# Optimization experiments

Hardware: AMD Instinct MI355X
Metric: run time of the kernel (lower is better)

The kernel has to match this reference:

```python
import jax, jax.numpy as jnp
import numpy as np

E, L, D, H, S, B = 8, 12, 768, 12, 512, 32
DIMS = [12, 8, 8, 8, 8, 12]
RANKS = [1, 8, 8, 8, 8, 8, 1]
ALPHA = 8.0


def setup_inputs() -> dict:
    key = jax.random.key(0)
    ks = iter(jax.random.split(key, 32))
    inp = {}
    inp['hidden_states'] = jax.random.normal(next(ks), (B, S, D), jnp.float32)
    inp['router_weights'] = jax.random.normal(next(ks), (D, E), jnp.float32)
    for pre in ('q', 'v'):
        for i in range(6):
            shp = (E, L, RANKS[i], DIMS[i], RANKS[i + 1])
            inp[f'{pre}_core{i}'] = jax.random.normal(next(ks), shp, jnp.float32) * 0.05
    for nm in ('Wq', 'Wk', 'Wv', 'Wo'):
        inp[nm] = jax.random.normal(next(ks), (L, D, D), jnp.float32) * 0.02
    for nm in ('bq', 'bk', 'bv', 'bo'):
        inp[nm] = jnp.zeros((L, D), jnp.float32)
    inp['ln_scale'] = jnp.ones((L, D), jnp.float32)
    inp['ln_bias'] = jnp.zeros((L, D), jnp.float32)
    return inp


def _layernorm(x, scale, bias, eps=1e-12):
    mu = x.mean(-1, keepdims=True)
    var = ((x - mu) ** 2).mean(-1, keepdims=True)
    return (x - mu) * jax.lax.rsqrt(var + eps) * scale + bias


def _tt_weights(cores):
    # cores[i]: [L, r_i, d_i, r_{i+1}]; chained TT contraction, vectorized over layers
    w = jnp.einsum('Lijk,Lklm,Lmno,Lopq,Lqrs,Lstu->Ljlnprt', *cores)
    return w.reshape(w.shape[0], D, D)  # [L, out, in] (matches torch weight.reshape)


def reference(hidden_states, router_weights,
              q_core0, q_core1, q_core2, q_core3, q_core4, q_core5,
              v_core0, v_core1, v_core2, v_core3, v_core4, v_core5,
              Wq, Wk, Wv, Wo, bq, bk, bv, bo, ln_scale, ln_bias):
    # routing: pool over sequence, softmax + argmax per sample
    pooled = hidden_states.mean(axis=1)                      # [B, D]
    probs = jax.nn.softmax(pooled @ router_weights, axis=-1)  # [B, E]
    idx = jnp.argmax(probs, axis=-1)                          # [B]
    e = idx[-1]
    qc = [c[e] for c in (q_core0, q_core1, q_core2, q_core3, q_core4, q_core5)]
    vc = [c[e] for c in (v_core0, v_core1, v_core2, v_core3, v_core4, v_core5)]
    Wq_a = Wq + ALPHA * _tt_weights(qc)  # [L, D, D]
    Wv_a = Wv + ALPHA * _tt_weights(vc)

    hd = D // H
    scale = 1.0 / jnp.sqrt(jnp.float32(hd))
    x = hidden_states
    for l in range(L):
        q = (x @ Wq_a[l].T + bq[l]).reshape(B, S, H, hd)
        k = (x @ Wk[l].T + bk[l]).reshape(B, S, H, hd)
        v = (x @ Wv_a[l].T + bv[l]).reshape(B, S, H, hd)
        scores = jnp.einsum('bqhd,bkhd->bhqk', q, k) * scale
        attn = jax.nn.softmax(scores, axis=-1)
        ctx = jnp.einsum('bhqk,bkhd->bqhd', attn, v).reshape(B, S, D)
        out = ctx @ Wo[l].T + bo[l]
        x = _layernorm(x + out, ln_scale[l], ln_bias[l])
    return x
```

## Files before the change

### kernel.cpp

```cpp
#include <hip/hip_runtime.h>
#include <hip/hip_bf16.h>
#include <stdint.h>

#define E_ 8
#define L_ 12
#define D_ 768
#define H_ 12
#define S_ 512
#define B_ 32
#define BS_ (B_*S_)

typedef __attribute__((ext_vector_type(4))) float floatx4;
typedef __attribute__((ext_vector_type(8))) __bf16 bf16x8;
typedef __attribute__((ext_vector_type(4))) __bf16 bf16x4;

__device__ __forceinline__ __bf16 f2bf(float f) {
  unsigned u = __builtin_bit_cast(unsigned, f);
  u += 0x7fffu + ((u >> 16) & 1u);
  unsigned short h = (unsigned short)(u >> 16);
  return __builtin_bit_cast(__bf16, h);
}

__device__ __forceinline__ float fexp2(float x) {
#if __has_builtin(__builtin_amdgcn_exp2f)
  return __builtin_amdgcn_exp2f(x);
#else
  return exp2f(x);
#endif
}

__device__ __forceinline__ void async16(const void* g, void* l) {
  __builtin_amdgcn_global_load_lds((__attribute__((address_space(1))) void*)g,
                                   (__attribute__((address_space(3))) void*)l,
                                   16, 0, 0);
}

__global__ void routing_pool_kernel(const float* __restrict__ hidden,
                                    float* __restrict__ partial) {
  const int blk = blockIdx.x;
  const int tid = threadIdx.x;
  const float* base = hidden + (size_t)(B_-1)*S_*D_ + (size_t)blk*8*D_;
  float acc[3] = {0.f, 0.f, 0.f};
  for (int s = 0; s < 8; ++s) {
#pragma unroll
    for (int i = 0; i < 3; ++i)
      acc[i] += base[(size_t)s*D_ + tid + i*256];
  }
#pragma unroll
  for (int i = 0; i < 3; ++i) partial[(size_t)blk*D_ + tid + i*256] = acc[i];
}

__global__ void routing_finish_kernel(const float* __restrict__ partial,
                                      const float* __restrict__ rw,
                                      int* __restrict__ e_out) {
  __shared__ float pooled[D_];
  __shared__ float logits[E_];
  int tid = threadIdx.x;
#pragma unroll
  for (int i = 0; i < 3; ++i) {
    int d = tid + i*256;
    float s = 0.f;
    for (int blk = 0; blk < 64; ++blk) s += partial[(size_t)blk*D_ + d];
    pooled[d] = s;
  }
  __syncthreads();
  if (tid < E_) {
    float s = 0.f;
    for (int d = 0; d < D_; ++d) s += pooled[d] * rw[d*E_ + tid];
    logits[tid] = s;
  }
  __syncthreads();
  if (tid == 0) {
    int best = 0; float bvv = logits[0];
    for (int e = 1; e < E_; ++e) if (logits[e] > bvv) { bvv = logits[e]; best = e; }
    e_out[0] = best;
  }
}

__global__ void convert_bf16_kernel(const float* __restrict__ src, __bf16* __restrict__ dst) {
  size_t i = ((size_t)blockIdx.x*256 + threadIdx.x)*8;
  __bf16 r[8];
#pragma unroll
  for (int j = 0; j < 8; ++j) r[j] = f2bf(src[i+j]);
  *(bf16x8*)(dst + i) = *(bf16x8*)r;
}

__global__ void convert_wk_kernel(const float* __restrict__ wk, __bf16* __restrict__ wqkv) {
  size_t i = ((size_t)blockIdx.x*256 + threadIdx.x)*8;
  int l = (int)(i / (D_*D_));
  int rem = (int)(i % (D_*D_));
  int n = rem / D_, k = rem % D_;
  __bf16 r[8];
#pragma unroll
  for (int j = 0; j < 8; ++j) r[j] = f2bf(wk[i+j]);
  *(bf16x8*)(wqkv + (size_t)l*2304*D_ + (size_t)(768+n)*D_ + k) = *(bf16x8*)r;
}

__global__ void tt_prep_kernel(
    const float* __restrict__ qc0, const float* __restrict__ qc1, const float* __restrict__ qc2,
    const float* __restrict__ qc3, const float* __restrict__ qc4, const float* __restrict__ qc5,
    const float* __restrict__ vc0, const float* __restrict__ vc1, const float* __restrict__ vc2,
    const float* __restrict__ vc3, const float* __restrict__ vc4, const float* __restrict__ vc5,
    const float* __restrict__ Wq, const float* __restrict__ Wv,
    const int* __restrict__ e_idx, __bf16* __restrict__ wqkv) {
  const int l = blockIdx.x;
  const int pre = blockIdx.y;
  const int z = blockIdx.z;
  const int tid = threadIdx.x;
  const int e = e_idx[0];
  const float* c0 = (pre ? vc0 : qc0) + (size_t)(e*L_ + l)*96;
  const float* c1 = (pre ? vc1 : qc1) + (size_t)(e*L_ + l)*512;
  const float* c2 = (pre ? vc2 : qc2) + (size_t)(e*L_ + l)*512;
  const float* c3 = (pre ? vc3 : qc3) + (size_t)(e*L_ + l)*512;
  const float* c4 = (pre ? vc4 : qc4) + (size_t)(e*L_ + l)*512;
  const float* c5 = (pre ? vc5 : qc5) + (size_t)(e*L_ + l)*96;
  __shared__ float M1[768];
  __shared__ float R2[768];
  __shared__ float M2[6144];
  __shared__ float Rm[6144];
  for (int idx = tid; idx < 768; idx += 256) {
    int j = idx >> 6, rem = idx & 63, l2 = rem >> 3, m = rem & 7;
    float s = 0.f;
    for (int k = 0; k < 8; ++k) s += c0[j*8 + k] * c1[k*64 + l2*8 + m];
    M1[idx] = s;
    int qq = idx / 96, rem2 = idx % 96, rr = rem2 / 12, t = rem2 % 12;
    float s2 = 0.f;
    for (int si = 0; si < 8; ++si) s2 += c4[qq*64 + rr*8 + si] * c5[si*12 + t];
    R2[idx] = s2;
  }
  __syncthreads();
  for (int idx = tid; idx < 6144; idx += 256) {
    int o = idx & 7, n = (idx >> 3) & 7, jl = idx >> 6;
    float s = 0.f;
    for (int m = 0; m < 8; ++m) s += M1[jl*8 + m] * c2[m*64 + n*8 + o];
    M2[idx] = s;
    int o2 = idx / 768, inp = idx % 768, p = inp / 96, rt = inp % 96;
    float s2 = 0.f;
    for (int qq = 0; qq < 8; ++qq) s2 += c3[o2*64 + p*8 + qq] * R2[qq*96 + rt];
    Rm[idx] = s2;
  }
  __syncthreads();
  const float* Wbase = (pre ? Wv : Wq) + (size_t)l*D_*D_;
  __bf16* dst = wqkv + (size_t)l*2304*D_ + (pre ? (size_t)1536*D_ : 0);
  for (int g = tid; g < 48*96; g += 256) {
    const int outr = z*48 + (g / 96);
    const int inp0 = (g % 96) * 8;
    float m2r[8];
#pragma unroll
    for (int o = 0; o < 8; ++o) m2r[o] = M2[outr*8 + o];
    float acc[8];
#pragma unroll
    for (int u = 0; u < 8; ++u) acc[u] = 0.f;
#pragma unroll
    for (int o = 0; o < 8; ++o) {
      float4 r0 = *(const float4*)&Rm[o*768 + inp0];
      float4 r1 = *(const float4*)&Rm[o*768 + inp0 + 4];
      acc[0] += m2r[o]*r0.x; acc[1] += m2r[o]*r0.y;
      acc[2] += m2r[o]*r0.z; acc[3] += m2r[o]*r0.w;
      acc[4] += m2r[o]*r1.x; acc[5] += m2r[o]*r1.y;
      acc[6] += m2r[o]*r1.z; acc[7] += m2r[o]*r1.w;
    }
    const float* wb = Wbase + (size_t)outr*768 + inp0;
    float4 w0 = *(const float4*)wb;
    float4 w1 = *(const float4*)(wb + 4);
    __bf16 r[8];
    r[0] = f2bf(w0.x + 8.f*acc[0]); r[1] = f2bf(w0.y + 8.f*acc[1]);
    r[2] = f2bf(w0.z + 8.f*acc[2]); r[3] = f2bf(w0.w + 8.f*acc[3]);
    r[4] = f2bf(w1.x + 8.f*acc[4]); r[5] = f2bf(w1.y + 8.f*acc[5]);
    r[6] = f2bf(w1.z + 8.f*acc[6]); r[7] = f2bf(w1.w + 8.f*acc[7]);
    *(bf16x8*)(dst + (size_t)outr*768 + inp0) = *(bf16x8*)r;
  }
}

#define SLOT_BYTES 28672
template<bool SPLITV>
__global__ __launch_bounds__(512, 2) void gemm_bt(
    const __bf16* __restrict__ A, const __bf16* __restrict__ Bw,
    const float* __restrict__ bq, const float* __restrict__ bk, const float* __restrict__ bvp,
    __bf16* __restrict__ outb, __bf16* __restrict__ vtout, int Nw) {
  __shared__ __align__(16) char lds[4*SLOT_BYTES];
  const int tid = threadIdx.x;
  const int w = tid >> 6, lane = tid & 63;
  const int quad = lane >> 4, l16 = lane & 15;
  const int wm = w >> 2, wn = w & 3;
  const size_t mblk = (size_t)blockIdx.y * 256;
  const size_t nblk = (size_t)blockIdx.x * 192;
  const __bf16* Ag = A + mblk * 768;
  const __bf16* Bg = Bw + nblk * 768;

  int a_goff[2], a_loff[2];
#pragma unroll
  for (int i = 0; i < 2; ++i) {
    int line = w*16 + i*8 + (lane >> 3);
    int s8 = (lane & 7) ^ (line & 7);
    int row = 2*line + (s8 >> 2);
    a_goff[i] = row*768 + (s8 & 3)*8;
    a_loff[i] = (w*16 + i*8)*128;
  }
  int b_goff[2], b_loff[2];
#pragma unroll
  for (int i = 0; i < 2; ++i) {
    int bl0 = (w < 4) ? (w*16 + i*8) : (64 + (w-4)*8);
    int line = bl0 + (lane >> 3);
    int s8 = (lane & 7) ^ (line & 7);
    int row = 2*line + (s8 >> 2);
    b_goff[i] = row*768 + (s8 & 3)*8;
    b_loff[i] = 16384 + bl0*128;
  }

  int a_foff[8], b_foff[3];
#pragma unroll
  for (int mf = 0; mf < 8; ++mf) {
    int r = wm*128 + mf*16 + l16;
    int line = r >> 1, s8 = (r & 1)*4 + quad, ph = s8 ^ (line & 7);
    a_foff[mf] = line*128 + ph*16;
  }
#pragma unroll
  for (int nf = 0; nf < 3; ++nf) {
    int r = wn*48 + nf*16 + l16;
    int line = r >> 1, s8 = (r & 1)*4 + quad, ph = s8 ^ (line & 7);
    b_foff[nf] = 16384 + line*128 + ph*16;
  }

  floatx4 acc[8][3];
#pragma unroll
  for (int mf = 0; mf < 8; ++mf)
#pragma unroll
    for (int nf = 0; nf < 3; ++nf) acc[mf][nf] = {0.f,0.f,0.f,0.f};

  auto STAGE = [&](int t) {
    const __bf16* Ab = Ag + t*32;
    const __bf16* Bb = Bg + t*32;
    char* ls = lds + (t & 3)*SLOT_BYTES;
    async16(Ab + a_goff[0], ls + a_loff[0]);
    async16(Ab + a_goff[1], ls + a_loff[1]);
    if (w < 4) {
      async16(Bb + b_goff[0], ls + b_loff[0]);
      async16(Bb + b_goff[1], ls + b_loff[1]);
    } else {
      async16(Bb + b_goff[0], ls + b_loff[0]);
    }
  };

  bf16x8 af[8], bfr[3];
  auto LOAD1 = [&](int u) {
    const char* ls = lds + (u & 3)*SLOT_BYTES;
#pragma unroll
    for (int nf = 0; nf < 3; ++nf) bfr[nf] = *(const bf16x8*)(ls + b_foff[nf]);
#pragma unroll
    for (int mf = 0; mf < 4; ++mf) af[mf] = *(const bf16x8*)(ls + a_foff[mf]);
  };
  auto LOAD2 = [&](int u) {
    const char* ls = lds + (u & 3)*SLOT_BYTES;
#pragma unroll
    for (int mf = 4; mf < 8; ++mf) af[mf] = *(const bf16x8*)(ls + a_foff[mf]);
  };
  auto MM = [&](int mf0) {
    __builtin_amdgcn_s_setprio(1);
#pragma unroll
    for (int mf = mf0; mf < mf0 + 4; ++mf)
#pragma unroll
      for (int nf = 0; nf < 3; ++nf)
        acc[mf][nf] = __builtin_amdgcn_mfma_f32_16x16x32_bf16(af[mf], bfr[nf], acc[mf][nf], 0, 0, 0);
    __builtin_amdgcn_s_setprio(0);
  };
  auto BAR = [&]() {
    __builtin_amdgcn_s_barrier();
    __builtin_amdgcn_sched_barrier(0);
  };

  STAGE(0); STAGE(1); STAGE(2);
  if (w < 4) asm volatile("s_waitcnt vmcnt(8)" ::: "memory");
  else       asm volatile("s_waitcnt vmcnt(6)" ::: "memory");
  BAR();

  for (int u = 0; u < 21; ++u) {
    LOAD1(u);
    BAR();
    MM(0);
    LOAD2(u);
    STAGE(u + 3);
    if (w < 4) asm volatile("s_waitcnt vmcnt(8)" ::: "memory");
    else       asm volatile("s_waitcnt vmcnt(6)" ::: "memory");
    BAR();
    MM(4);
  }
  LOAD1(21);
  BAR();
  MM(0);
  LOAD2(21);
  if (w < 4) asm volatile("s_waitcnt vmcnt(4)" ::: "memory");
  else       asm volatile("s_waitcnt vmcnt(3)" ::: "memory");
  BAR();
  MM(4);
  LOAD1(22);
  BAR();
  MM(0);
  LOAD2(22);
  asm volatile("s_waitcnt vmcnt(0)" ::: "memory");
  BAR();
  MM(4);
  LOAD1(23);
  BAR();
  MM(0);
  LOAD2(23);
  BAR();
  MM(4);

  if (SPLITV && blockIdx.x >= 8) {
#pragma unroll
    for (int nf = 0; nf < 3; ++nf) {
      const int vcol = (int)nblk - 1536 + wn*48 + nf*16 + l16;
      const int h = vcol >> 6, d = vcol & 63;
      const float bval = bvp[vcol];
#pragma unroll
      for (int mf = 0; mf < 8; ++mf) {
        const int mrow = (int)mblk + wm*128 + mf*16 + quad*4;
        const int b = mrow >> 9, s = mrow & 511;
        __bf16 pr[4];
#pragma unroll
        for (int r = 0; r < 4; ++r) pr[r] = f2bf(acc[mf][nf][r] + bval);
        *(bf16x4*)(vtout + (size_t)((b*H_ + h)*64 + d)*S_ + s) = *(bf16x4*)pr;
      }
    }
    return;
  }
  const float* bias = bq;
  if (SPLITV) bias = (blockIdx.x < 4) ? bq : bk;
  float bval[3]; int ncol[3];
#pragma unroll
  for (int nf = 0; nf < 3; ++nf) {
    ncol[nf] = (int)nblk + wn*48 + nf*16 + l16;
    int bc = ncol[nf]; if (bc >= 768) bc -= 768;
    bval[nf] = bias[bc];
  }
#pragma unroll
  for (int mf = 0; mf < 8; ++mf) {
#pragma unroll
    for (int nf = 0; nf < 3; ++nf) {
#pragma unroll
      for (int r = 0; r < 4; ++r) {
        const int mrow = (int)mblk + wm*128 + mf*16 + quad*4 + r;
        outb[(size_t)mrow*Nw + ncol[nf]] = f2bf(acc[mf][nf][r] + bval[nf]);
      }
    }
  }
}

#define PSTR 72
__global__ __launch_bounds__(256) void flash_kernel(const __bf16* __restrict__ qkv,
                                                    const __bf16* __restrict__ vt,
                                                    __bf16* __restrict__ ctx) {
  __shared__ __align__(16) __bf16 Qs[64*PSTR];
  __shared__ __align__(16) __bf16 Ks[64*PSTR];
  __shared__ __align__(16) __bf16 Vts[64*PSTR];
  __shared__ __align__(16) __bf16 Ps[64*PSTR];
  const int tid = threadIdx.x;
  const int w = tid >> 6, lane = tid & 63;
  const int quad = lane >> 4, l16 = lane & 15;
  const int n = blockIdx.x;
  const int bh = (n >> 6)*8 + (n & 7);
  const int q0 = ((n >> 3) & 7) * 64;
  const int b = bh / H_, h = bh % H_;
  const float SCL = 0.125f * 1.44269504f;

  const int row0 = tid >> 3,        seg0 = tid & 7;
  const int row1 = (256 + tid) >> 3, seg1 = tid & 7;

  bf16x8 ka[2], va[2], kb[2], vb[2];
  ka[0] = *(const bf16x8*)(qkv + (size_t)(b*S_ + row0)*2304 + 768 + h*64 + seg0*8);
  va[0] = *(const bf16x8*)(vt  + (size_t)(bh*64 + row0)*S_ + seg0*8);
  ka[1] = *(const bf16x8*)(qkv + (size_t)(b*S_ + row1)*2304 + 768 + h*64 + seg1*8);
  va[1] = *(const bf16x8*)(vt  + (size_t)(bh*64 + row1)*S_ + seg1*8);

  {
    bf16x8 v0 = *(const bf16x8*)(qkv + (size_t)(b*S_ + q0 + row0)*2304 + h*64 + seg0*8);
    bf16x8 v1 = *(const bf16x8*)(qkv + (size_t)(b*S_ + q0 + row1)*2304 + h*64 + seg1*8);
    *(bf16x8*)&Qs[row0*PSTR + seg0*8] = v0;
    *(bf16x8*)&Qs[row1*PSTR + seg1*8] = v1;
  }

  floatx4 acc_o[4];
#pragma unroll
  for (int jd = 0; jd < 4; ++jd) acc_o[jd] = {0.f,0.f,0.f,0.f};
  float m_prev = -__builtin_inff();
  float l_part = 0.f;

  auto STEP = [&](int kt, bf16x8* ck, bf16x8* cv, bf16x8* nk, bf16x8* nv, bool pf) {
    asm volatile("s_waitcnt lgkmcnt(0)" ::: "memory");
    __builtin_amdgcn_s_barrier();
    __builtin_amdgcn_sched_barrier(0);
    *(bf16x8*)&Ks[row0*PSTR + seg0*8]  = ck[0];
    *(bf16x8*)&Vts[row0*PSTR + seg0*8] = cv[0];
    *(bf16x8*)&Ks[row1*PSTR + seg1*8]  = ck[1];
    *(bf16x8*)&Vts[row1*PSTR + seg1*8] = cv[1];
    if (pf) {
      nk[0] = *(const bf16x8*)(qkv + (size_t)(b*S_ + (kt+1)*64 + row0)*2304 + 768 + h*64 + seg0*8);
      nv[0] = *(const bf16x8*)(vt  + (size_t)(bh*64 + row0)*S_ + (kt+1)*64 + seg0*8);
      nk[1] = *(const bf16x8*)(qkv + (size_t)(b*S_ + (kt+1)*64 + row1)*2304 + 768 + h*64 + seg1*8);
      nv[1] = *(const bf16x8*)(vt  + (size_t)(bh*64 + row1)*S_ + (kt+1)*64 + seg1*8);
    }
    asm volatile("s_waitcnt lgkmcnt(0)" ::: "memory");
    __builtin_amdgcn_s_barrier();
    __builtin_amdgcn_sched_barrier(0);

    floatx4 sacc[4];
#pragma unroll
    for (int i = 0; i < 4; ++i) sacc[i] = {0.f,0.f,0.f,0.f};
    __builtin_amdgcn_s_setprio(1);
#pragma unroll
    for (int kk = 0; kk < 64; kk += 32) {
      bf16x8 bq_ = *(const bf16x8*)&Qs[(w*16 + l16)*PSTR + kk + quad*8];
#pragma unroll
      for (int i = 0; i < 4; ++i) {
        bf16x8 ak = *(const bf16x8*)&Ks[(i*16 + l16)*PSTR + kk + quad*8];
        sacc[i] = __builtin_amdgcn_mfma_f32_16x16x32_bf16(ak, bq_, sacc[i], 0, 0, 0);
      }
    }
    __builtin_amdgcn_s_setprio(0);
#pragma unroll
    for (int i = 0; i < 4; ++i)
#pragma unroll
      for (int r = 0; r < 4; ++r) sacc[i][r] *= SCL;
    float mloc = sacc[0][0];
#pragma unroll
    for (int i = 0; i < 4; ++i)
#pragma unroll
      for (int r = 0; r < 4; ++r) mloc = fmaxf(mloc, sacc[i][r]);
    mloc = fmaxf(mloc, __shfl_xor(mloc, 16));
    mloc = fmaxf(mloc, __shfl_xor(mloc, 32));
    float mnew = fmaxf(m_prev, mloc);
    float alpha = fexp2(m_prev - mnew);
    m_prev = mnew;
    float rsum = 0.f;
#pragma unroll
    for (int i = 0; i < 4; ++i) {
      __bf16 pr[4];
#pragma unroll
      for (int r = 0; r < 4; ++r) {
        float p = fexp2(sacc[i][r] - mnew);
        rsum += p;
        pr[r] = f2bf(p);
      }
      *(bf16x4*)&Ps[(w*16 + l16)*PSTR + i*16 + quad*4] = *(bf16x4*)pr;
    }
    l_part = l_part*alpha + rsum;
    float ab[4];
#pragma unroll
    for (int r = 0; r < 4; ++r) ab[r] = __shfl(alpha, quad*4 + r);
#pragma unroll
    for (int jd = 0; jd < 4; ++jd)
#pragma unroll
      for (int r = 0; r < 4; ++r) acc_o[jd][r] *= ab[r];
#pragma unroll
    for (int kk = 0; kk < 64; kk += 32) {
      bf16x8 ap = *(const bf16x8*)&Ps[(w*16 + l16)*PSTR + kk + quad*8];
      __builtin_amdgcn_s_setprio(1);
#pragma unroll
      for (int jd = 0; jd < 4; ++jd) {
        bf16x8 bv_ = *(const bf16x8*)&Vts[(jd*16 + l16)*PSTR + kk + quad*8];
        acc_o[jd] = __builtin_amdgcn_mfma_f32_16x16x32_bf16(ap, bv_, acc_o[jd], 0, 0, 0);
      }
      __builtin_amdgcn_s_setprio(0);
    }
  };

#pragma unroll
  for (int kt2 = 0; kt2 < 8; kt2 += 2) {
    STEP(kt2,     ka, va, kb, vb, true);
    STEP(kt2 + 1, kb, vb, ka, va, kt2 + 1 < 7);
  }

  float l_tot = l_part;
  l_tot += __shfl_xor(l_tot, 16);
  l_tot += __shfl_xor(l_tot, 32);
  float lb[4];
#pragma unroll
  for (int r = 0; r < 4; ++r) lb[r] = __shfl(l_tot, quad*4 + r);
#pragma unroll
  for (int jd = 0; jd < 4; ++jd) {
    const int d = jd*16 + l16;
#pragma unroll
    for (int r = 0; r < 4; ++r) {
      const int q = q0 + w*16 + quad*4 + r;
      ctx[(size_t)(b*S_ + q)*D_ + h*64 + d] = f2bf(acc_o[jd][r] / lb[r]);
    }
  }
}

template<bool FIRST, bool LAST>
__global__ __launch_bounds__(256) void ln_kernel(const float* __restrict__ residf,
                                                 __bf16* xb,
                                                 const __bf16* __restrict__ proj,
                                                 const float* __restrict__ gamma,
                                                 const float* __restrict__ beta,
                                                 float* __restrict__ xoutf) {
  const int tid = threadIdx.x;
  const int w = tid >> 6, lane = tid & 63;
  const int row = blockIdx.x*4 + w;
  const size_t base = (size_t)row * D_;
  const int c0 = lane*8;
  const bool has2 = lane < 32;
  const int c1 = 512 + lane*8;

  float v0[8], v1[8];
  {
    bf16x8 p0 = *(const bf16x8*)(proj + base + c0);
    if (FIRST) {
      float4 a = *(const float4*)(residf + base + c0);
      float4 bq4 = *(const float4*)(residf + base + c0 + 4);
      v0[0]=a.x+(float)p0[0]; v0[1]=a.y+(float)p0[1]; v0[2]=a.z+(float)p0[2]; v0[3]=a.w+(float)p0[3];
      v0[4]=bq4.x+(float)p0[4]; v0[5]=bq4.y+(float)p0[5]; v0[6]=bq4.z+(float)p0[6]; v0[7]=bq4.w+(float)p0[7];
    } else {
      bf16x8 r0 = *(const bf16x8*)(xb + base + c0);
#pragma unroll
      for (int j = 0; j < 8; ++j) v0[j] = (float)r0[j] + (float)p0[j];
    }
    if (has2) {
      bf16x8 p1 = *(const bf16x8*)(proj + base + c1);
      if (FIRST) {
        float4 a = *(const float4*)(residf + base + c1);
        float4 bq4 = *(const float4*)(residf + base + c1 + 4);
        v1[0]=a.x+(float)p1[0]; v1[1]=a.y+(float)p1[1]; v1[2]=a.z+(float)p1[2]; v1[3]=a.w+(float)p1[3];
        v1[4]=bq4.x+(float)p1[4]; v1[5]=bq4.y+(float)p1[5]; v1[6]=bq4.z+(float)p1[6]; v1[7]=bq4.w+(float)p1[7];
      } else {
        bf16x8 r1 = *(const bf16x8*)(xb + base + c1);
#pragma unroll
        for (int j = 0; j < 8; ++j) v1[j] = (float)r1[j] + (float)p1[j];
      }
    } else {
#pragma unroll
      for (int j = 0; j < 8; ++j) v1[j] = 0.f;
    }
  }
  float s = 0.f;
#pragma unroll
  for (int j = 0; j < 8; ++j) s += v0[j] + v1[j];
#pragma unroll
  for (int off = 32; off; off >>= 1) s += __shfl_xor(s, off);
  const float mu = s * (1.f/768.f);
  float q = 0.f;
#pragma unroll
  for (int j = 0; j < 8; ++j) { float d0 = v0[j]-mu; q += d0*d0; }
  if (has2) {
#pragma unroll
    for (int j = 0; j < 8; ++j) { float d1 = v1[j]-mu; q += d1*d1; }
  }
#pragma unroll
  for (int off = 32; off; off >>= 1) q += __shfl_xor(q, off);
  const float rs = rsqrtf(q * (1.f/768.f) + 1e-12f);

  {
    float4 g0 = *(const float4*)(gamma + c0);
    float4 g1 = *(const float4*)(gamma + c0 + 4);
    float4 b0 = *(const float4*)(beta + c0);
    float4 b1 = *(const float4*)(beta + c0 + 4);
    float o[8];
    o[0]=(v0[0]-mu)*rs*g0.x+b0.x; o[1]=(v0[1]-mu)*rs*g0.y+b0.y;
    o[2]=(v0[2]-mu)*rs*g0.z+b0.z; o[3]=(v0[3]-mu)*rs*g0.w+b0.w;
    o[4]=(v0[4]-mu)*rs*g1.x+b1.x; o[5]=(v0[5]-mu)*rs*g1.y+b1.y;
    o[6]=(v0[6]-mu)*rs*g1.z+b1.z; o[7]=(v0[7]-mu)*rs*g1.w+b1.w;
    if (LAST) {
      *(float4*)(xoutf + base + c0)     = {o[0],o[1],o[2],o[3]};
      *(float4*)(xoutf + base + c0 + 4) = {o[4],o[5],o[6],o[7]};
    } else {
      __bf16 ob[8];
#pragma unroll
      for (int j = 0; j < 8; ++j) ob[j] = f2bf(o[j]);
      *(bf16x8*)(xb + base + c0) = *(bf16x8*)ob;
    }
  }
  if (has2) {
    float4 g0 = *(const float4*)(gamma + c1);
    float4 g1 = *(const float4*)(gamma + c1 + 4);
    float4 b0 = *(const float4*)(beta + c1);
    float4 b1 = *(const float4*)(beta + c1 + 4);
    float o[8];
    o[0]=(v1[0]-mu)*rs*g0.x+b0.x; o[1]=(v1[1]-mu)*rs*g0.y+b0.y;
    o[2]=(v1[2]-mu)*rs*g0.z+b0.z; o[3]=(v1[3]-mu)*rs*g0.w+b0.w;
    o[4]=(v1[4]-mu)*rs*g1.x+b1.x; o[5]=(v1[5]-mu)*rs*g1.y+b1.y;
    o[6]=(v1[6]-mu)*rs*g1.z+b1.z; o[7]=(v1[7]-mu)*rs*g1.w+b1.w;
    if (LAST) {
      *(float4*)(xoutf + base + c1)     = {o[0],o[1],o[2],o[3]};
      *(float4*)(xoutf + base + c1 + 4) = {o[4],o[5],o[6],o[7]};
    } else {
      __bf16 ob[8];
#pragma unroll
      for (int j = 0; j < 8; ++j) ob[j] = f2bf(o[j]);
      *(bf16x8*)(xb + base + c1) = *(bf16x8*)ob;
    }
  }
}

extern "C" void kernel_launch(void* const* d_in, const int* in_sizes, int n_in,
                              void* d_out, int out_size, void* d_ws, size_t ws_size,
                              hipStream_t stream) {
  const float* hidden = (const float*)d_in[0];
  const float* router = (const float*)d_in[1];
  const float* qc[6]; const float* vc[6];
  for (int i = 0; i < 6; ++i) qc[i] = (const float*)d_in[2+i];
  for (int i = 0; i < 6; ++i) vc[i] = (const float*)d_in[8+i];
  const float* Wq = (const float*)d_in[14];
  const float* Wk = (const float*)d_in[15];
  const float* Wv = (const float*)d_in[16];
  const float* Wo = (const float*)d_in[17];
  const float* bq = (const float*)d_in[18];
  const float* bk = (const float*)d_in[19];
  const float* bv = (const float*)d_in[20];
  const float* bo = (const float*)d_in[21];
  const float* lns = (const float*)d_in[22];
  const float* lnb = (const float*)d_in[23];
  float* out = (float*)d_out;

  char* ws = (char*)d_ws;
  size_t off = 0;
  auto alloc = [&](size_t bytes) -> void* {
    off = (off + 255) & ~(size_t)255;
    void* p = ws + off; off += bytes; return p;
  };
  int*    e_idx = (int*)   alloc(4);
  float*  rpart = (float*) alloc((size_t)64*D_*4);
  __bf16* xbf   = (__bf16*)alloc((size_t)BS_*D_*2);
  __bf16* qkv   = (__bf16*)alloc((size_t)BS_*2304*2);
  __bf16* vt    = (__bf16*)alloc((size_t)B_*H_*64*S_*2);
  __bf16* ctx   = (__bf16*)alloc((size_t)BS_*D_*2);
  __bf16* projb = (__bf16*)alloc((size_t)BS_*D_*2);
  __bf16* wqkv  = (__bf16*)alloc((size_t)L_*2304*D_*2);
  __bf16* wobf  = (__bf16*)alloc((size_t)L_*D_*D_*2);
  (void)ws_size; (void)in_sizes; (void)n_in; (void)out_size;

  routing_pool_kernel<<<64, 256, 0, stream>>>(hidden, rpart);
  routing_finish_kernel<<<1, 256, 0, stream>>>(rpart, router, e_idx);
  convert_bf16_kernel<<<(BS_*D_)/2048, 256, 0, stream>>>(hidden, xbf);
  tt_prep_kernel<<<dim3(L_, 2, 16), 256, 0, stream>>>(qc[0],qc[1],qc[2],qc[3],qc[4],qc[5],
                                                      vc[0],vc[1],vc[2],vc[3],vc[4],vc[5],
                                                      Wq, Wv, e_idx, wqkv);
  convert_wk_kernel<<<(L_*D_*D_)/2048, 256, 0, stream>>>(Wk, wqkv);
  convert_bf16_kernel<<<(L_*D_*D_)/2048, 256, 0, stream>>>(Wo, wobf);

  for (int l = 0; l < L_; ++l) {
    gemm_bt<true><<<dim3(12,64), 512, 0, stream>>>(xbf, wqkv + (size_t)l*2304*D_,
        bq + l*D_, bk + l*D_, bv + l*D_, qkv, vt, 2304);
    flash_kernel<<<3072, 256, 0, stream>>>(qkv, vt, ctx);
    gemm_bt<false><<<dim3(4,64), 512, 0, stream>>>(ctx, wobf + (size_t)l*D_*D_,
        bo + l*D_, nullptr, nullptr, projb, nullptr, 768);
    if (l == 0)
      ln_kernel<true,false><<<BS_/4, 256, 0, stream>>>(hidden, xbf, projb,
          lns + l*D_, lnb + l*D_, nullptr);
    else if (l == L_-1)
      ln_kernel<false,true><<<BS_/4, 256, 0, stream>>>(nullptr, xbf, projb,
          lns + l*D_, lnb + l*D_, out);
    else
      ln_kernel<false,false><<<BS_/4, 256, 0, stream>>>(nullptr, xbf, projb,
          lns + l*D_, lnb + l*D_, nullptr);
  }
}
```

Measured before the change: 2.446 ms.

## Keep Q in registers and skip online-softmax rescale when max barely grows

The flash attention kernel now holds Q fragments in registers instead of shared memory. It skips the running-max rescale of the output accumulator unless some row's max grows by more than a threshold (FA4-style lazy rescaling). The change also packs P to bf16 with v_cvt_pk_bf16_f32, uses incrementing prefetch pointers, multiplies by a reciprocal at the end, and sets launch bounds for 4 blocks per CU. The intent is to cut LDS traffic, exp and multiply work, and raise occupancy, at the cost of exponents up to 2^10 before normalization and a different rounding mode for the conversion.

Result: faster. 2.254 ms (-7.9%).

```diff
diff --git a/kernel.cpp b/kernel.cpp
--- a/kernel.cpp
+++ b/kernel.cpp
@@ -13,12 +13,19 @@
 typedef __attribute__((ext_vector_type(4))) float floatx4;
 typedef __attribute__((ext_vector_type(8))) __bf16 bf16x8;
 typedef __attribute__((ext_vector_type(4))) __bf16 bf16x4;
+typedef __attribute__((ext_vector_type(2))) unsigned uintx2;
 
 __device__ __forceinline__ __bf16 f2bf(float f) {
   unsigned u = __builtin_bit_cast(unsigned, f);
   u += 0x7fffu + ((u >> 16) & 1u);
   unsigned short h = (unsigned short)(u >> 16);
   return __builtin_bit_cast(__bf16, h);
+}
+
+__device__ __forceinline__ unsigned cvtpk_bf16(float lo, float hi) {
+  unsigned r;
+  asm("v_cvt_pk_bf16_f32 %0, %1, %2" : "=v"(r) : "v"(lo), "v"(hi));
+  return r;
 }
 
 __device__ __forceinline__ float fexp2(float x) {
@@ -348,10 +355,9 @@
 }
 
 #define PSTR 72
-__global__ __launch_bounds__(256) void flash_kernel(const __bf16* __restrict__ qkv,
-                                                    const __bf16* __restrict__ vt,
-                                                    __bf16* __restrict__ ctx) {
-  __shared__ __align__(16) __bf16 Qs[64*PSTR];
+__global__ __launch_bounds__(256, 4) void flash_kernel(const __bf16* __restrict__ qkv,
+                                                       const __bf16* __restrict__ vt,
+                                                       __bf16* __restrict__ ctx) {
   __shared__ __align__(16) __bf16 Ks[64*PSTR];
   __shared__ __align__(16) __bf16 Vts[64*PSTR];
   __shared__ __align__(16) __bf16 Ps[64*PSTR];
@@ -364,7 +370,7 @@
   const int b = bh / H_, h = bh % H_;
   const float SCL = 0.125f * 1.44269504f;
 
-  const int row0 = tid >> 3,        seg0 = tid & 7;
+  const int row0 = tid >> 3,         seg0 = tid & 7;
   const int row1 = (256 + tid) >> 3, seg1 = tid & 7;
 
   bf16x8 ka[2], va[2], kb[2], vb[2];
@@ -373,12 +379,17 @@
   ka[1] = *(const bf16x8*)(qkv + (size_t)(b*S_ + row1)*2304 + 768 + h*64 + seg1*8);
   va[1] = *(const bf16x8*)(vt  + (size_t)(bh*64 + row1)*S_ + seg1*8);
 
+  bf16x8 qf0, qf1;
   {
-    bf16x8 v0 = *(const bf16x8*)(qkv + (size_t)(b*S_ + q0 + row0)*2304 + h*64 + seg0*8);
-    bf16x8 v1 = *(const bf16x8*)(qkv + (size_t)(b*S_ + q0 + row1)*2304 + h*64 + seg1*8);
-    *(bf16x8*)&Qs[row0*PSTR + seg0*8] = v0;
-    *(bf16x8*)&Qs[row1*PSTR + seg1*8] = v1;
-  }
+    const __bf16* qrow = qkv + (size_t)(b*S_ + q0 + w*16 + l16)*2304 + h*64 + quad*8;
+    qf0 = *(const bf16x8*)qrow;
+    qf1 = *(const bf16x8*)(qrow + 32);
+  }
+
+  const __bf16* kp0 = qkv + (size_t)(b*S_ + 64 + row0)*2304 + 768 + h*64 + seg0*8;
+  const __bf16* kp1 = qkv + (size_t)(b*S_ + 64 + row1)*2304 + 768 + h*64 + seg1*8;
+  const __bf16* vp0 = vt  + (size_t)(bh*64 + row0)*S_ + 64 + seg0*8;
+  const __bf16* vp1 = vt  + (size_t)(bh*64 + row1)*S_ + 64 + seg1*8;
 
   floatx4 acc_o[4];
 #pragma unroll
@@ -386,7 +397,7 @@
   float m_prev = -__builtin_inff();
   float l_part = 0.f;
 
-  auto STEP = [&](int kt, bf16x8* ck, bf16x8* cv, bf16x8* nk, bf16x8* nv, bool pf) {
+  auto STEP = [&](bf16x8* ck, bf16x8* cv, bf16x8* nk, bf16x8* nv, bool pf) {
     asm volatile("s_waitcnt lgkmcnt(0)" ::: "memory");
     __builtin_amdgcn_s_barrier();
     __builtin_amdgcn_sched_barrier(0);
@@ -395,10 +406,10 @@
     *(bf16x8*)&Ks[row1*PSTR + seg1*8]  = ck[1];
     *(bf16x8*)&Vts[row1*PSTR + seg1*8] = cv[1];
     if (pf) {
-      nk[0] = *(const bf16x8*)(qkv + (size_t)(b*S_ + (kt+1)*64 + row0)*2304 + 768 + h*64 + seg0*8);
-      nv[0] = *(const bf16x8*)(vt  + (size_t)(bh*64 + row0)*S_ + (kt+1)*64 + seg0*8);
-      nk[1] = *(const bf16x8*)(qkv + (size_t)(b*S_ + (kt+1)*64 + row1)*2304 + 768 + h*64 + seg1*8);
-      nv[1] = *(const bf16x8*)(vt  + (size_t)(bh*64 + row1)*S_ + (kt+1)*64 + seg1*8);
+      nk[0] = *(const bf16x8*)kp0; kp0 += 64*2304;
+      nv[0] = *(const bf16x8*)vp0; vp0 += 64;
+      nk[1] = *(const bf16x8*)kp1; kp1 += 64*2304;
+      nv[1] = *(const bf16x8*)vp1; vp1 += 64;
     }
     asm volatile("s_waitcnt lgkmcnt(0)" ::: "memory");
     __builtin_amdgcn_s_barrier();
@@ -410,7 +421,7 @@
     __builtin_amdgcn_s_setprio(1);
 #pragma unroll
     for (int kk = 0; kk < 64; kk += 32) {
-      bf16x8 bq_ = *(const bf16x8*)&Qs[(w*16 + l16)*PSTR + kk + quad*8];
+      bf16x8 bq_ = kk ? qf1 : qf0;
 #pragma unroll
       for (int i = 0; i < 4; ++i) {
         bf16x8 ak = *(const bf16x8*)&Ks[(i*16 + l16)*PSTR + kk + quad*8];
@@ -429,29 +440,33 @@
       for (int r = 0; r < 4; ++r) mloc = fmaxf(mloc, sacc[i][r]);
     mloc = fmaxf(mloc, __shfl_xor(mloc, 16));
     mloc = fmaxf(mloc, __shfl_xor(mloc, 32));
-    float mnew = fmaxf(m_prev, mloc);
-    float alpha = fexp2(m_prev - mnew);
-    m_prev = mnew;
+    const bool resc = !__all(mloc <= m_prev + 10.f);
+    float mnew = m_prev;
+    if (resc) mnew = fmaxf(m_prev, mloc);
     float rsum = 0.f;
 #pragma unroll
     for (int i = 0; i < 4; ++i) {
-      __bf16 pr[4];
-#pragma unroll
-      for (int r = 0; r < 4; ++r) {
-        float p = fexp2(sacc[i][r] - mnew);
-        rsum += p;
-        pr[r] = f2bf(p);
-      }
-      *(bf16x4*)&Ps[(w*16 + l16)*PSTR + i*16 + quad*4] = *(bf16x4*)pr;
-    }
-    l_part = l_part*alpha + rsum;
-    float ab[4];
-#pragma unroll
-    for (int r = 0; r < 4; ++r) ab[r] = __shfl(alpha, quad*4 + r);
-#pragma unroll
-    for (int jd = 0; jd < 4; ++jd)
-#pragma unroll
-      for (int r = 0; r < 4; ++r) acc_o[jd][r] *= ab[r];
+      float p0 = fexp2(sacc[i][0] - mnew);
+      float p1 = fexp2(sacc[i][1] - mnew);
+      float p2 = fexp2(sacc[i][2] - mnew);
+      float p3 = fexp2(sacc[i][3] - mnew);
+      rsum += (p0 + p1) + (p2 + p3);
+      uintx2 pk = { cvtpk_bf16(p0, p1), cvtpk_bf16(p2, p3) };
+      *(uintx2*)&Ps[(w*16 + l16)*PSTR + i*16 + quad*4] = pk;
+    }
+    if (resc) {
+      float alpha = fexp2(m_prev - mnew);
+      m_prev = mnew;
+      l_part *= alpha;
+      float ab[4];
+#pragma unroll
+      for (int r = 0; r < 4; ++r) ab[r] = __shfl(alpha, quad*4 + r);
+#pragma unroll
+      for (int jd = 0; jd < 4; ++jd)
+#pragma unroll
+        for (int r = 0; r < 4; ++r) acc_o[jd][r] *= ab[r];
+    }
+    l_part += rsum;
 #pragma unroll
     for (int kk = 0; kk < 64; kk += 32) {
       bf16x8 ap = *(const bf16x8*)&Ps[(w*16 + l16)*PSTR + kk + quad*8];
@@ -467,8 +482,8 @@
 
 #pragma unroll
   for (int kt2 = 0; kt2 < 8; kt2 += 2) {
-    STEP(kt2,     ka, va, kb, vb, true);
-    STEP(kt2 + 1, kb, vb, ka, va, kt2 + 1 < 7);
+    STEP(ka, va, kb, vb, true);
+    STEP(kb, vb, ka, va, kt2 + 1 < 7);
   }
 
   float l_tot = l_part;
@@ -476,14 +491,14 @@
   l_tot += __shfl_xor(l_tot, 32);
   float lb[4];
 #pragma unroll
-  for (int r = 0; r < 4; ++r) lb[r] = __shfl(l_tot, quad*4 + r);
+  for (int r = 0; r < 4; ++r) lb[r] = 1.f / __shfl(l_tot, quad*4 + r);
 #pragma unroll
   for (int jd = 0; jd < 4; ++jd) {
     const int d = jd*16 + l16;
 #pragma unroll
     for (int r = 0; r < 4; ++r) {
       const int q = q0 + w*16 + quad*4 + r;
-      ctx[(size_t)(b*S_ + q)*D_ + h*64 + d] = f2bf(acc_o[jd][r] / lb[r]);
+      ctx[(size_t)(b*S_ + q)*D_ + h*64 + d] = f2bf(acc_o[jd][r] * lb[r]);
     }
   }
 }
```
